# Performance work log

Hardware: AMD Instinct MI355X
Metric: run time of the kernel (lower is better)

The kernel has to match this reference:

```python
import math
import jax, jax.numpy as jnp
import numpy as np

D, H, L, DFF, V = 512, 8, 6, 2048, 32000
B, S = 2, 2048
PAD = 1


def _layernorm(x, g, b, eps=1e-5):
    m = x.mean(-1, keepdims=True)
    v = ((x - m) ** 2).mean(-1, keepdims=True)
    return (x - m) / jnp.sqrt(v + eps) * g + b


def _mha(qx, kx, w, b, mask, h=H):
    # w: [4, D, D] (q,k,v,out), b: [4, D]; mask broadcastable to [B,1,Sq,Sk]
    bs, sq, d = qx.shape
    dk = d // h
    def proj(x, i):
        return (x @ w[i] + b[i]).reshape(bs, -1, h, dk).transpose(0, 2, 1, 3)
    q, k, v = proj(qx, 0), proj(kx, 1), proj(kx, 2)
    scores = jnp.einsum('bhqd,bhkd->bhqk', q, k) / math.sqrt(dk)
    scores = jnp.where(mask, scores, -jnp.inf)
    attn = jax.nn.softmax(scores, axis=-1)
    out = jnp.einsum('bhqk,bhkd->bhqd', attn, v).transpose(0, 2, 1, 3).reshape(bs, sq, d)
    return out @ w[3] + b[3]


def _ff(x, w1, b1, w2, b2):
    return jax.nn.relu(x @ w1 + b1) @ w2 + b2


def _sinusoidal_pe(max_len, d):
    pos = np.arange(max_len)[:, None].astype(np.float64)
    div = np.exp(np.arange(0, d, 2) * (-math.log(10000.0) / d))
    pe = np.zeros((max_len, d), np.float32)
    pe[:, 0::2] = np.sin(pos * div)
    pe[:, 1::2] = np.cos(pos * div)
    return jnp.asarray(pe[None])  # [1, max_len, d]


def setup_inputs() -> dict:
    key = jax.random.key(0)
    ks = iter(jax.random.split(key, 32))
    def w(shape):
        return jax.random.normal(next(ks), shape, jnp.float32) * 0.02
    inp = {
        'src': jax.random.randint(next(ks), (B, S), 2, V),
        'tgt': jax.random.randint(next(ks), (B, S), 2, V),
        'src_emb': w((V, D)),
        'tgt_emb': w((V, D)),
        'pe': _sinusoidal_pe(S, D),
        'enc_attn_w': w((L, 4, D, D)), 'enc_attn_b': jnp.zeros((L, 4, D)),
        'enc_ff_w1': w((L, D, DFF)), 'enc_ff_b1': jnp.zeros((L, DFF)),
        'enc_ff_w2': w((L, DFF, D)), 'enc_ff_b2': jnp.zeros((L, D)),
        'enc_ln_g': jnp.ones((L, 2, D)), 'enc_ln_b': jnp.zeros((L, 2, D)),
        'dec_self_w': w((L, 4, D, D)), 'dec_self_b': jnp.zeros((L, 4, D)),
        'dec_src_w': w((L, 4, D, D)), 'dec_src_b': jnp.zeros((L, 4, D)),
        'dec_ff_w1': w((L, D, DFF)), 'dec_ff_b1': jnp.zeros((L, DFF)),
        'dec_ff_w2': w((L, DFF, D)), 'dec_ff_b2': jnp.zeros((L, D)),
        'dec_ln_g': jnp.ones((L, 3, D)), 'dec_ln_b': jnp.zeros((L, 3, D)),
        'ln_g': jnp.ones((D,)), 'ln_b': jnp.zeros((D,)),
        'fc_w': w((D, V)), 'fc_b': jnp.zeros((V,)),
    }
    return inp


def reference(src, tgt, src_emb, tgt_emb, pe,
              enc_attn_w, enc_attn_b, enc_ff_w1, enc_ff_b1, enc_ff_w2, enc_ff_b2,
              enc_ln_g, enc_ln_b,
              dec_self_w, dec_self_b, dec_src_w, dec_src_b,
              dec_ff_w1, dec_ff_b1, dec_ff_w2, dec_ff_b2, dec_ln_g, dec_ln_b,
              ln_g, ln_b, fc_w, fc_b):
    s_len, t_len = src.shape[1], tgt.shape[1]
    src_mask = (src != PAD)[:, None, None, :]                      # [B,1,1,Ss]
    tril = jnp.tril(jnp.ones((t_len, t_len), bool))
    tgt_mask = (tgt != PAD)[:, None, None, :] & tril[None, None]   # [B,1,St,St]

    x = src_emb[src] + pe[:, :s_len]
    for l in range(L):
        x2 = _layernorm(x, enc_ln_g[l, 0], enc_ln_b[l, 0])
        x = x + _mha(x2, x2, enc_attn_w[l], enc_attn_b[l], src_mask)
        x2 = _layernorm(x, enc_ln_g[l, 1], enc_ln_b[l, 1])
        x = x + _ff(x2, enc_ff_w1[l], enc_ff_b1[l], enc_ff_w2[l], enc_ff_b2[l])
    memory = x

    y = tgt_emb[tgt] + pe[:, :t_len]
    for l in range(L):
        y2 = _layernorm(y, dec_ln_g[l, 0], dec_ln_b[l, 0])
        y = y + _mha(y2, y2, dec_self_w[l], dec_self_b[l], tgt_mask)
        y2 = _layernorm(y, dec_ln_g[l, 1], dec_ln_b[l, 1])
        y = y + _mha(y2, memory, dec_src_w[l], dec_src_b[l], src_mask)
        y2 = _layernorm(y, dec_ln_g[l, 2], dec_ln_b[l, 2])
        y = y + _ff(y2, dec_ff_w1[l], dec_ff_b1[l], dec_ff_w2[l], dec_ff_b2[l])

    return _layernorm(y, ln_g, ln_b) @ fc_w + fc_b  # [B, St, V]
```

## Files before the change

kernel.cpp:

```cpp
#include <hip/hip_runtime.h>
#include <math.h>

#define D_MODEL 512
#define NHEAD   8
#define NLAYER  6
#define DFF_    2048
#define VOCAB   32000
#define BATCH   2
#define SEQ     2048
#define NTOK    (BATCH*SEQ)
#define PAD_ID  1

typedef __attribute__((ext_vector_type(8))) short s16x8;
typedef __attribute__((ext_vector_type(4))) float f32x4;
typedef unsigned short u16;
typedef unsigned int   u32;
typedef unsigned long long u64;

__device__ __forceinline__ u16 f2bf(float x) {
  u32 u = __builtin_bit_cast(u32, x);
  u += 0x7FFFu + ((u >> 16) & 1u);
  return (u16)(u >> 16);
}

__device__ __forceinline__ float exp2i(float x) {
  float r; asm("v_exp_f32 %0, %1" : "=v"(r) : "v"(x)); return r;
}

__device__ __forceinline__ void gload16(const void* g, void* l) {
  __builtin_amdgcn_global_load_lds(
      (const __attribute__((address_space(1))) u32*)g,
      (__attribute__((address_space(3))) u32*)l, 16, 0, 0);
}

#define CEXP 0.1803368802f

__global__ __launch_bounds__(256) void embed_kernel(
    const int* __restrict__ tok, const float* __restrict__ emb,
    const float* __restrict__ pe, float* __restrict__ out)
{
  const int total = NTOK * D_MODEL;
  for (int i = blockIdx.x * 256 + threadIdx.x; i < total; i += gridDim.x * 256) {
    int t = i >> 9;
    int d = i & 511;
    int s = t & (SEQ - 1);
    out[i] = emb[(size_t)tok[t] * D_MODEL + d] + pe[(size_t)s * D_MODEL + d];
  }
}

__global__ __launch_bounds__(64) void padmask_kernel(
    const int* __restrict__ tok, u64* __restrict__ pm)
{
  int b = blockIdx.y, t = blockIdx.x;
  int lane = threadIdx.x;
  u64 m = __ballot(tok[(size_t)b * SEQ + t * 64 + lane] != PAD_ID);
  if (lane == 0) pm[b * (SEQ / 64) + t] = m;
}

__global__ __launch_bounds__(256) void ln_kernel(
    const float* __restrict__ x, const float* __restrict__ g,
    const float* __restrict__ bb, u16* __restrict__ y)
{
  __shared__ float red[8];
  const size_t row = blockIdx.x;
  const float* xr = x + row * D_MODEL;
  u16* yr = y + row * D_MODEL;
  const int t = threadIdx.x;
  float a0 = xr[t], a1 = xr[t + 256];
  float s = a0 + a1;
  #pragma unroll
  for (int o = 32; o > 0; o >>= 1) s += __shfl_down(s, o, 64);
  int wv = t >> 6, ln = t & 63;
  if (ln == 0) red[wv] = s;
  __syncthreads();
  if (t == 0) red[4] = red[0] + red[1] + red[2] + red[3];
  __syncthreads();
  float mean = red[4] * (1.0f / D_MODEL);
  float d0 = a0 - mean, d1 = a1 - mean;
  float vs = d0 * d0 + d1 * d1;
  #pragma unroll
  for (int o = 32; o > 0; o >>= 1) vs += __shfl_down(vs, o, 64);
  if (ln == 0) red[wv] = vs;
  __syncthreads();
  if (t == 0) red[5] = red[0] + red[1] + red[2] + red[3];
  __syncthreads();
  float inv = rsqrtf(red[5] * (1.0f / D_MODEL) + 1e-5f);
  yr[t]       = f2bf(d0 * inv * g[t]       + bb[t]);
  yr[t + 256] = f2bf(d1 * inv * g[t + 256] + bb[t + 256]);
}

__global__ __launch_bounds__(256) void cvtbf_kernel(
    const float* __restrict__ s, u16* __restrict__ d, int n)
{
  int i = (blockIdx.x * 256 + threadIdx.x) * 8;
  if (i >= n) return;
  float4 a = *(const float4*)&s[i];
  float4 b = *(const float4*)&s[i + 4];
  u32 p0 = (u32)f2bf(a.x) | ((u32)f2bf(a.y) << 16);
  u32 p1 = (u32)f2bf(a.z) | ((u32)f2bf(a.w) << 16);
  u32 p2 = (u32)f2bf(b.x) | ((u32)f2bf(b.y) << 16);
  u32 p3 = (u32)f2bf(b.z) | ((u32)f2bf(b.w) << 16);
  uint4 o; o.x = p0; o.y = p1; o.z = p2; o.w = p3;
  *(uint4*)&d[i] = o;
}

__global__ __launch_bounds__(256) void tconv_kernel(
    const float* __restrict__ src, u16* __restrict__ dst, int K, int N)
{
  __shared__ float tile[64][65];
  const size_t z = blockIdx.z;
  src += z * (size_t)K * N;
  dst += z * (size_t)K * N;
  const int n0 = blockIdx.x * 64, k0 = blockIdx.y * 64;
  const int t = threadIdx.x;
  const int cr = t >> 4, cc = (t & 15) * 4;
  #pragma unroll
  for (int it = 0; it < 4; ++it) {
    int kr = cr + it * 16;
    float4 v = *(const float4*)&src[(size_t)(k0 + kr) * N + n0 + cc];
    tile[kr][cc] = v.x; tile[kr][cc + 1] = v.y; tile[kr][cc + 2] = v.z; tile[kr][cc + 3] = v.w;
  }
  __syncthreads();
  #pragma unroll
  for (int it = 0; it < 4; ++it) {
    int nr = cr + it * 16;
    u32 lo = (u32)f2bf(tile[cc + 0][nr]) | ((u32)f2bf(tile[cc + 1][nr]) << 16);
    u32 hi = (u32)f2bf(tile[cc + 2][nr]) | ((u32)f2bf(tile[cc + 3][nr]) << 16);
    uint2 pk; pk.x = lo; pk.y = hi;
    *(uint2*)&dst[(size_t)(n0 + nr) * K + k0 + cc] = pk;
  }
}

template<int MODE, int BM, int BN, int MAP>
__global__ __launch_bounds__(256, 2) void mm_kernel(
    const u16* __restrict__ A, const u16* __restrict__ Wt,
    const float* __restrict__ bias, const float* __restrict__ res,
    void* __restrict__ Cout, u16* __restrict__ vtOut,
    int M, int N, int K,
    long long wStride, long long bStride, long long cStride)
{
  constexpr int MI = BM / 32;
  constexpr int NI = BN / 32;
  __shared__ u16 sh[(BM + BN) * 64];
  u16* As = sh;
  u16* Bs = sh + BM * 64;
  const int z = blockIdx.z;
  size_t wOff, bOff;
  if (MAP == 1) {
    wOff = (size_t)(z >> 1) * 4 * 262144 + (size_t)(1 + (z & 1)) * 262144;
    bOff = (size_t)(z >> 1) * 4 * 512 + (size_t)(1 + (z & 1)) * 512;
  } else {
    wOff = (size_t)z * wStride;
    bOff = (size_t)z * bStride;
  }
  Wt += wOff;
  bias += bOff;
  const int bm = blockIdx.y * BM, bn = blockIdx.x * BN;
  const int tid = threadIdx.x, lane = tid & 63, w = tid >> 6;
  const int wm = w >> 1, wn = w & 1;
  const int l15 = lane & 15, l4 = lane >> 4;
  const int wrow0 = wm * (BM / 2), wcol0 = wn * (BN / 2);
  const u16* aBase = A  + (size_t)bm * K;
  const u16* bBase = Wt + (size_t)bn * K;
  f32x4 acc[MI][NI] = {};

  for (int k0 = 0; k0 < K; k0 += 64) {
    #pragma unroll
    for (int i = 0; i < BM / 32; ++i) {
      int lin = i * 256 + tid;
      int r = lin >> 3, sp = lin & 7;
      gload16(aBase + (size_t)r * K + k0 + ((sp ^ (r & 7)) * 8), &As[(i * 256 + w * 64) * 8]);
    }
    #pragma unroll
    for (int i = 0; i < BN / 32; ++i) {
      int lin = i * 256 + tid;
      int r = lin >> 3, sp = lin & 7;
      gload16(bBase + (size_t)r * K + k0 + ((sp ^ (r & 7)) * 8), &Bs[(i * 256 + w * 64) * 8]);
    }
    __syncthreads();
    #pragma unroll
    for (int ks = 0; ks < 2; ++ks) {
      s16x8 af[MI], bf[NI];
      #pragma unroll
      for (int mi = 0; mi < MI; ++mi) {
        int rr = wrow0 + mi * 16 + l15;
        af[mi] = *(const s16x8*)&As[(rr << 6) + (((ks * 4 + l4) ^ (rr & 7)) << 3)];
      }
      #pragma unroll
      for (int ni = 0; ni < NI; ++ni) {
        int rr = wcol0 + ni * 16 + l15;
        bf[ni] = *(const s16x8*)&Bs[(rr << 6) + (((ks * 4 + l4) ^ (rr & 7)) << 3)];
      }
      #pragma unroll
      for (int mi = 0; mi < MI; ++mi)
        #pragma unroll
        for (int ni = 0; ni < NI; ++ni)
          acc[mi][ni] = __builtin_amdgcn_mfma_f32_16x16x32_bf16(af[mi], bf[ni], acc[mi][ni], 0, 0, 0);
    }
    __syncthreads();
  }

  const bool vpath = (MODE == 4 && z == 2) || (MODE == 5 && (z & 1) == 1);
  if (vpath) {
    u16* TT = sh;
    #pragma unroll
    for (int mi = 0; mi < MI; ++mi)
      #pragma unroll
      for (int ni = 0; ni < NI; ++ni)
        #pragma unroll
        for (int r = 0; r < 4; ++r) {
          int rowl = wrow0 + mi * 16 + l4 * 4 + r;
          int coll = wcol0 + ni * 16 + l15;
          TT[coll * 72 + rowl] = f2bf(acc[mi][ni][r] + bias[bn + coll]);
        }
    __syncthreads();
    const int b = bm >> 11, s0loc = bm & 2047, h = bn >> 6;
    const int layer = (MODE == 5) ? (z >> 1) : 0;
    u16* vbase = vtOut + (size_t)layer * ((size_t)NTOK * D_MODEL)
               + ((size_t)(b * NHEAD + h) * 64) * SEQ;
    int d = tid >> 2, sc = (tid & 3) * 16;
    s16x8 v0 = *(const s16x8*)&TT[d * 72 + sc];
    s16x8 v1 = *(const s16x8*)&TT[d * 72 + sc + 8];
    *(s16x8*)(vbase + (size_t)d * SEQ + s0loc + sc) = v0;
    *(s16x8*)(vbase + (size_t)d * SEQ + s0loc + sc + 8) = v1;
    return;
  }

  const int zi = (MAP == 1) ? (z >> 1) : z;
  #pragma unroll
  for (int ni = 0; ni < NI; ++ni) {
    int col = bn + wcol0 + ni * 16 + l15;
    float bb = bias[col];
    #pragma unroll
    for (int mi = 0; mi < MI; ++mi) {
      #pragma unroll
      for (int r = 0; r < 4; ++r) {
        int row = bm + wrow0 + mi * 16 + l4 * 4 + r;
        size_t off = (size_t)zi * cStride + (size_t)row * N + col;
        float v = acc[mi][ni][r] + bb;
        if (MODE == 1) v += res[(size_t)row * N + col];
        if (MODE == 3) v = fmaxf(v, 0.0f);
        if (MODE <= 1) ((float*)Cout)[off] = v;
        else           ((u16*)Cout)[off] = f2bf(v);
      }
    }
  }
}

template<int CAUSAL>
__global__ __launch_bounds__(256, 2) void fattn_kernel(
    const u16* __restrict__ Qg, const u16* __restrict__ Kg,
    const u16* __restrict__ Vt, const u64* __restrict__ padm,
    u16* __restrict__ Og)
{
  __shared__ u16 Ks[2][128 * 64];
  __shared__ u16 Vs[2][64 * 128];
  __shared__ u16 Ps[4][16 * 128];
  const int qtile = CAUSAL ? (int)(gridDim.x - 1 - blockIdx.x) : (int)blockIdx.x;
  const int qt = qtile * 64;
  const int h = blockIdx.y, b = blockIdx.z;
  const int tid = threadIdx.x, lane = tid & 63, w = tid >> 6;
  const int l15 = lane & 15, l4 = lane >> 4;
  const int hoff = h * 64;
  const u16* Kbase = Kg + (size_t)(b * SEQ) * D_MODEL + hoff;
  const u16* Vbase = Vt + (size_t)(b * NHEAD + h) * 64 * SEQ;
  const u64* pmb = padm + b * (SEQ / 64);

  s16x8 aq[2];
  {
    const u16* qp = Qg + (size_t)(b * SEQ + qt + w * 16 + l15) * D_MODEL + hoff + l4 * 8;
    aq[0] = *(const s16x8*)qp;
    aq[1] = *(const s16x8*)(qp + 32);
  }

  f32x4 oacc[4] = {};
  float mrow[4] = {-1e30f, -1e30f, -1e30f, -1e30f};
  float lrow[4] = {0.f, 0.f, 0.f, 0.f};
  const int nt = CAUSAL ? (qt >> 7) + 1 : SEQ / 128;

  #define STAGE(KV0, BUF)                                                              \
    {                                                                                  \
      _Pragma("unroll")                                                                \
      for (int it = 0; it < 4; ++it) {                                                 \
        int lin = it * 256 + tid;                                                      \
        int rr = lin >> 3, sp = lin & 7;                                               \
        gload16(Kbase + (size_t)((KV0) + rr) * D_MODEL + ((sp ^ (rr & 7)) * 8),        \
                &Ks[BUF][(it * 256 + w * 64) * 8]);                                    \
      }                                                                                \
      _Pragma("unroll")                                                                \
      for (int it = 0; it < 4; ++it) {                                                 \
        int lin = it * 256 + tid;                                                      \
        int rr = lin >> 4, ko = lin & 15;                                              \
        gload16(Vbase + (size_t)rr * SEQ + (KV0) + ((ko ^ (rr & 15)) * 8),             \
                &Vs[BUF][(it * 256 + w * 64) * 8]);                                    \
      }                                                                                \
    }

  STAGE(0, 0);
  __syncthreads();

  for (int kt = 0; kt < nt; ++kt) {
    const int kv0 = kt * 128;
    const int cur = kt & 1;
    if (kt + 1 < nt) STAGE(kv0 + 128, cur ^ 1);

    f32x4 sac[8] = {};
    #pragma unroll
    for (int ks = 0; ks < 2; ++ks)
      #pragma unroll
      for (int jn = 0; jn < 8; ++jn) {
        int rr = jn * 16 + l15;
        s16x8 bk = *(const s16x8*)&Ks[cur][(rr << 6) + (((ks * 4 + l4) ^ (rr & 7)) << 3)];
        sac[jn] = __builtin_amdgcn_mfma_f32_16x16x32_bf16(aq[ks], bk, sac[jn], 0, 0, 0);
      }

    const u64 m0 = pmb[(kv0 >> 6)];
    const u64 m1 = pmb[(kv0 >> 6) + 1];
    const bool lastC = CAUSAL && (kt == nt - 1);
    if (((m0 & m1) != ~0ull) || lastC) {
      #pragma unroll
      for (int jn = 0; jn < 8; ++jn) {
        int kvg = kv0 + jn * 16 + l15;
        u64 mm = (jn < 4) ? m0 : m1;
        bool okp = (mm >> ((jn & 3) * 16 + l15)) & 1;
        #pragma unroll
        for (int r = 0; r < 4; ++r) {
// ... 55 lines not shown
    }
    __syncthreads();
  }
  #undef STAGE

  float inv[4];
  #pragma unroll
  for (int r = 0; r < 4; ++r) inv[r] = 1.0f / lrow[r];
  #pragma unroll
  for (int jn = 0; jn < 4; ++jn)
    #pragma unroll
    for (int r = 0; r < 4; ++r)
      Og[(size_t)(b * SEQ + qt + w * 16 + l4 * 4 + r) * D_MODEL + hoff + jn * 16 + l15] =
          f2bf(oacc[jn][r] * inv[r]);
}

extern "C" void kernel_launch(void* const* d_in, const int* in_sizes, int n_in,
                              void* d_out, int out_size, void* d_ws, size_t ws_size,
                              hipStream_t stream)
{
  const int*   src        = (const int*)  d_in[0];
  const int*   tgt        = (const int*)  d_in[1];
  const float* src_emb    = (const float*)d_in[2];
  const float* tgt_emb    = (const float*)d_in[3];
  const float* pe         = (const float*)d_in[4];
  const float* enc_attn_w = (const float*)d_in[5];
  const float* enc_attn_b = (const float*)d_in[6];
  const float* enc_ff_w1  = (const float*)d_in[7];
  const float* enc_ff_b1  = (const float*)d_in[8];
  const float* enc_ff_w2  = (const float*)d_in[9];
  const float* enc_ff_b2  = (const float*)d_in[10];
  const float* enc_ln_g   = (const float*)d_in[11];
  const float* enc_ln_bb  = (const float*)d_in[12];
  const float* dec_self_w = (const float*)d_in[13];
  const float* dec_self_b = (const float*)d_in[14];
  const float* dec_src_w  = (const float*)d_in[15];
  const float* dec_src_b  = (const float*)d_in[16];
  const float* dec_ff_w1  = (const float*)d_in[17];
  const float* dec_ff_b1  = (const float*)d_in[18];
  const float* dec_ff_w2  = (const float*)d_in[19];
  const float* dec_ff_b2  = (const float*)d_in[20];
  const float* dec_ln_g   = (const float*)d_in[21];
  const float* dec_ln_bb  = (const float*)d_in[22];
  const float* fin_ln_g   = (const float*)d_in[23];
  const float* fin_ln_b   = (const float*)d_in[24];
  const float* fc_w       = (const float*)d_in[25];
  const float* fc_b       = (const float*)d_in[26];
  float* out = (float*)d_out;

  const size_t DD = (size_t)D_MODEL * D_MODEL;
  const size_t FD = (size_t)D_MODEL * DFF_;
  const size_t TD = (size_t)NTOK * D_MODEL;

  char* ob = (char*)d_out;
  size_t off = 0;
  auto alloco = [&](size_t bytes) { void* p = ob + off; off += (bytes + 255) & ~(size_t)255; return p; };
  u16* wt_enc_attn = (u16*)alloco(24 * DD * 2);
  u16* wt_dec_self = (u16*)alloco(24 * DD * 2);
  u16* wt_dec_src  = (u16*)alloco(24 * DD * 2);
  u16* wt_enc_ff1  = (u16*)alloco(6 * FD * 2);
  u16* wt_enc_ff2  = (u16*)alloco(6 * FD * 2);
  u16* wt_dec_ff1  = (u16*)alloco(6 * FD * 2);
  u16* wt_dec_ff2  = (u16*)alloco(6 * FD * 2);
  u16* qb   = (u16*)alloco(2 * TD * 2);
  u16* kb   = qb + TD;
  u16* vtb  = (u16*)alloco(TD * 2);
  u16* aob  = (u16*)alloco(TD * 2);
  u16* hbb  = (u16*)alloco((size_t)NTOK * DFF_ * 2);
  u16* memb = (u16*)alloco(TD * 2);
  u16* ckb  = (u16*)alloco(6 * TD * 2);
  u16* cvtb = (u16*)alloco(6 * TD * 2);

  char* wsb = (char*)d_ws;
  u16*   fcwt = (u16*)wsb;
  size_t wo = ((size_t)VOCAB * D_MODEL * 2 + 255) & ~(size_t)255;
  float* xe  = (float*)(wsb + wo); wo += TD * 4;
  float* yd  = (float*)(wsb + wo); wo += TD * 4;
  u16*   x2b = (u16*)(wsb + wo);   wo += TD * 2;
  u64*   pmS = (u64*)(wsb + wo);   wo += 1024;
  u64*   pmT = (u64*)(wsb + wo);

  dim3 blk(256);
  dim3 gN512(8, 64, 1), gQKV(8, 64, 3), gCKV(8, 64, 12);
  dim3 gFF1(16, 32, 1), gFF2(8, 64, 1), gFC(250, 32, 1);
  dim3 gAttn(SEQ / 64, NHEAD, BATCH);
  dim3 gPM(SEQ / 64, BATCH);
  const long long llDD = (long long)DD, llTD = (long long)TD;

  padmask_kernel<<<gPM, dim3(64), 0, stream>>>(src, pmS);
  padmask_kernel<<<gPM, dim3(64), 0, stream>>>(tgt, pmT);
  tconv_kernel<<<dim3(8, 8, 24), blk, 0, stream>>>(enc_attn_w, wt_enc_attn, 512, 512);
  tconv_kernel<<<dim3(8, 8, 24), blk, 0, stream>>>(dec_self_w, wt_dec_self, 512, 512);
  tconv_kernel<<<dim3(8, 8, 24), blk, 0, stream>>>(dec_src_w,  wt_dec_src,  512, 512);
  tconv_kernel<<<dim3(32, 8, 6), blk, 0, stream>>>(enc_ff_w1, wt_enc_ff1, 512, 2048);
  tconv_kernel<<<dim3(8, 32, 6), blk, 0, stream>>>(enc_ff_w2, wt_enc_ff2, 2048, 512);
  tconv_kernel<<<dim3(32, 8, 6), blk, 0, stream>>>(dec_ff_w1, wt_dec_ff1, 512, 2048);
  tconv_kernel<<<dim3(8, 32, 6), blk, 0, stream>>>(dec_ff_w2, wt_dec_ff2, 2048, 512);
  tconv_kernel<<<dim3(500, 8, 1), blk, 0, stream>>>(fc_w, fcwt, 512, VOCAB);

  embed_kernel<<<dim3(2048), blk, 0, stream>>>(src, src_emb, pe, xe);
  for (int l = 0; l < NLAYER; ++l) {
    ln_kernel<<<dim3(NTOK), blk, 0, stream>>>(xe, enc_ln_g + (size_t)(l * 2 + 0) * D_MODEL,
                                              enc_ln_bb + (size_t)(l * 2 + 0) * D_MODEL, x2b);
    mm_kernel<4, 64, 64, 0><<<gQKV, blk, 0, stream>>>(x2b, wt_enc_attn + (size_t)l * 4 * DD,
        enc_attn_b + (size_t)l * 4 * D_MODEL, nullptr, qb, vtb, NTOK, 512, 512, llDD, D_MODEL, llTD);
    fattn_kernel<0><<<gAttn, blk, 0, stream>>>(qb, kb, vtb, pmS, aob);
    mm_kernel<1, 64, 64, 0><<<gN512, blk, 0, stream>>>(aob, wt_enc_attn + (size_t)(l * 4 + 3) * DD,
        enc_attn_b + (size_t)(l * 4 + 3) * D_MODEL, xe, xe, nullptr, NTOK, 512, 512, 0, 0, 0);
    ln_kernel<<<dim3(NTOK), blk, 0, stream>>>(xe, enc_ln_g + (size_t)(l * 2 + 1) * D_MODEL,
                                              enc_ln_bb + (size_t)(l * 2 + 1) * D_MODEL, x2b);
    mm_kernel<3, 128, 128, 0><<<gFF1, blk, 0, stream>>>(x2b, wt_enc_ff1 + (size_t)l * FD,
        enc_ff_b1 + (size_t)l * DFF_, nullptr, hbb, nullptr, NTOK, DFF_, 512, 0, 0, 0);
    mm_kernel<1, 64, 64, 0><<<gFF2, blk, 0, stream>>>(hbb, wt_enc_ff2 + (size_t)l * FD,
        enc_ff_b2 + (size_t)l * D_MODEL, xe, xe, nullptr, NTOK, 512, DFF_, 0, 0, 0);
  }
  cvtbf_kernel<<<dim3(1024), blk, 0, stream>>>(xe, memb, NTOK * D_MODEL);

  mm_kernel<5, 64, 64, 1><<<gCKV, blk, 0, stream>>>(memb, wt_dec_src, dec_src_b, nullptr,
      ckb, cvtb, NTOK, 512, 512, 0, 0, llTD);

  embed_kernel<<<dim3(2048), blk, 0, stream>>>(tgt, tgt_emb, pe, yd);
  for (int l = 0; l < NLAYER; ++l) {
    const u16* Ws = wt_dec_self + (size_t)l * 4 * DD;
    const u16* Wc = wt_dec_src + (size_t)l * 4 * DD;
    const float* bs  = dec_self_b + (size_t)l * 4 * D_MODEL;
    const float* bcb = dec_src_b + (size_t)l * 4 * D_MODEL;
    ln_kernel<<<dim3(NTOK), blk, 0, stream>>>(yd, dec_ln_g + (size_t)(l * 3 + 0) * D_MODEL,
                                              dec_ln_bb + (size_t)(l * 3 + 0) * D_MODEL, x2b);
    mm_kernel<4, 64, 64, 0><<<gQKV, blk, 0, stream>>>(x2b, Ws, bs, nullptr, qb, vtb,
                                                      NTOK, 512, 512, llDD, D_MODEL, llTD);
    fattn_kernel<1><<<gAttn, blk, 0, stream>>>(qb, kb, vtb, pmT, aob);
    mm_kernel<1, 64, 64, 0><<<gN512, blk, 0, stream>>>(aob, Ws + 3 * DD, bs + 3 * D_MODEL, yd, yd,
                                                       nullptr, NTOK, 512, 512, 0, 0, 0);
    ln_kernel<<<dim3(NTOK), blk, 0, stream>>>(yd, dec_ln_g + (size_t)(l * 3 + 1) * D_MODEL,
                                              dec_ln_bb + (size_t)(l * 3 + 1) * D_MODEL, x2b);
    mm_kernel<2, 64, 64, 0><<<gN512, blk, 0, stream>>>(x2b, Wc, bcb, nullptr, qb, nullptr,
                                                       NTOK, 512, 512, 0, 0, 0);
    fattn_kernel<0><<<gAttn, blk, 0, stream>>>(qb, ckb + (size_t)l * TD, cvtb + (size_t)l * TD,
                                               pmS, aob);
    mm_kernel<1, 64, 64, 0><<<gN512, blk, 0, stream>>>(aob, Wc + 3 * DD, bcb + 3 * D_MODEL, yd, yd,
                                                       nullptr, NTOK, 512, 512, 0, 0, 0);
    ln_kernel<<<dim3(NTOK), blk, 0, stream>>>(yd, dec_ln_g + (size_t)(l * 3 + 2) * D_MODEL,
                                              dec_ln_bb + (size_t)(l * 3 + 2) * D_MODEL, x2b);
    mm_kernel<3, 128, 128, 0><<<gFF1, blk, 0, stream>>>(x2b, wt_dec_ff1 + (size_t)l * FD,
        dec_ff_b1 + (size_t)l * DFF_, nullptr, hbb, nullptr, NTOK, DFF_, 512, 0, 0, 0);
    mm_kernel<1, 64, 64, 0><<<gFF2, blk, 0, stream>>>(hbb, wt_dec_ff2 + (size_t)l * FD,
        dec_ff_b2 + (size_t)l * D_MODEL, yd, yd, nullptr, NTOK, 512, DFF_, 0, 0, 0);
  }

  ln_kernel<<<dim3(NTOK), blk, 0, stream>>>(yd, fin_ln_g, fin_ln_b, x2b);
  mm_kernel<0, 128, 128, 0><<<gFC, blk, 0, stream>>>(x2b, fcwt, fc_b, nullptr, out, nullptr,
                                                     NTOK, VOCAB, 512, 0, 0, 0);

  (void)in_sizes; (void)n_in; (void)out_size; (void)ws_size;
}
```

Baseline: 2.516 ms.

## Fuse LayerNorm into following GEMMs and batch setup kernels

```diff
diff --git a/kernel.cpp b/kernel.cpp
--- a/kernel.cpp
+++ b/kernel.cpp
@@ -35,10 +35,15 @@
 
 #define CEXP 0.1803368802f
 
-__global__ __launch_bounds__(256) void embed_kernel(
-    const int* __restrict__ tok, const float* __restrict__ emb,
-    const float* __restrict__ pe, float* __restrict__ out)
-{
+__global__ __launch_bounds__(256) void embed2_kernel(
+    const int* __restrict__ src, const int* __restrict__ tgt,
+    const float* __restrict__ se, const float* __restrict__ te,
+    const float* __restrict__ pe, float* __restrict__ xe, float* __restrict__ yd)
+{
+  const int z = blockIdx.y;
+  const int* tok = z ? tgt : src;
+  const float* emb = z ? te : se;
+  float* out = z ? yd : xe;
   const int total = NTOK * D_MODEL;
   for (int i = blockIdx.x * 256 + threadIdx.x; i < total; i += gridDim.x * 256) {
     int t = i >> 9;
@@ -48,9 +53,13 @@
   }
 }
 
-__global__ __launch_bounds__(64) void padmask_kernel(
-    const int* __restrict__ tok, u64* __restrict__ pm)
-{
+__global__ __launch_bounds__(64) void padmask2_kernel(
+    const int* __restrict__ src, const int* __restrict__ tgt,
+    u64* __restrict__ pmS, u64* __restrict__ pmT)
+{
+  const int z = blockIdx.z;
+  const int* tok = z ? tgt : src;
+  u64* pm = z ? pmT : pmS;
   int b = blockIdx.y, t = blockIdx.x;
   int lane = threadIdx.x;
   u64 m = __ballot(tok[(size_t)b * SEQ + t * 64 + lane] != PAD_ID);
@@ -89,28 +98,14 @@
   yr[t + 256] = f2bf(d1 * inv * g[t + 256] + bb[t + 256]);
 }
 
-__global__ __launch_bounds__(256) void cvtbf_kernel(
-    const float* __restrict__ s, u16* __restrict__ d, int n)
-{
-  int i = (blockIdx.x * 256 + threadIdx.x) * 8;
-  if (i >= n) return;
-  float4 a = *(const float4*)&s[i];
-  float4 b = *(const float4*)&s[i + 4];
-  u32 p0 = (u32)f2bf(a.x) | ((u32)f2bf(a.y) << 16);
-  u32 p1 = (u32)f2bf(a.z) | ((u32)f2bf(a.w) << 16);
-  u32 p2 = (u32)f2bf(b.x) | ((u32)f2bf(b.y) << 16);
-  u32 p3 = (u32)f2bf(b.z) | ((u32)f2bf(b.w) << 16);
-  uint4 o; o.x = p0; o.y = p1; o.z = p2; o.w = p3;
-  *(uint4*)&d[i] = o;
-}
-
-__global__ __launch_bounds__(256) void tconv_kernel(
-    const float* __restrict__ src, u16* __restrict__ dst, int K, int N)
+__global__ __launch_bounds__(256) void tconv2_kernel(
+    const float* __restrict__ s0, const float* __restrict__ s1,
+    u16* __restrict__ d0, u16* __restrict__ d1, int zsplit, int K, int N)
 {
   __shared__ float tile[64][65];
-  const size_t z = blockIdx.z;
-  src += z * (size_t)K * N;
-  dst += z * (size_t)K * N;
+  const int z = blockIdx.z;
+  const float* src = (z < zsplit) ? s0 + (size_t)z * K * N : s1 + (size_t)(z - zsplit) * K * N;
+  u16* dst = (z < zsplit) ? d0 + (size_t)z * K * N : d1 + (size_t)(z - zsplit) * K * N;
   const int n0 = blockIdx.x * 64, k0 = blockIdx.y * 64;
   const int t = threadIdx.x;
   const int cr = t >> 4, cc = (t & 15) * 4;
@@ -128,6 +123,139 @@
     u32 hi = (u32)f2bf(tile[cc + 2][nr]) | ((u32)f2bf(tile[cc + 3][nr]) << 16);
     uint2 pk; pk.x = lo; pk.y = hi;
     *(uint2*)&dst[(size_t)(n0 + nr) * K + k0 + cc] = pk;
+  }
+}
+
+template<int MODE>
+__global__ __launch_bounds__(256, 2) void mmln_kernel(
+    const float* __restrict__ Xf, const float* __restrict__ lng,
+    const float* __restrict__ lnb, const u16* __restrict__ Wt,
+    const float* __restrict__ bias, u16* __restrict__ Cout,
+    u16* __restrict__ vtOut, int N,
+    long long wStride, long long bStride, long long cStride)
+{
+  __shared__ u16 Ap[64 * 512];
+  __shared__ u16 Bs[2][64 * 64];
+  const int z = blockIdx.z;
+  Wt   += (size_t)z * wStride;
+  bias += (size_t)z * bStride;
+  const int bm = blockIdx.y * 64, bn = blockIdx.x * 64;
+  const int tid = threadIdx.x, lane = tid & 63, w = tid >> 6;
+  const int wm = w >> 1, wn = w & 1;
+  const int l15 = lane & 15, l4 = lane >> 4;
+  const u16* bBase = Wt + (size_t)bn * 512;
+
+  #define STAGE_B(K0, BUF)                                                    \
+    { _Pragma("unroll")                                                       \
+      for (int i = 0; i < 2; ++i) {                                           \
+        int lin = i * 256 + tid;                                              \
+        int rr2 = lin >> 3, sp = lin & 7;                                     \
+        gload16(bBase + (size_t)rr2 * 512 + (K0) + ((sp ^ (rr2 & 7)) * 8),    \
+                &Bs[BUF][(i * 256 + w * 64) * 8]);                            \
+      } }
+
+  STAGE_B(0, 0);
+
+  const int r = tid >> 2, q = tid & 3;
+  const float* xrow = Xf + (size_t)(bm + r) * 512 + q * 128;
+  float sum = 0.f, ss = 0.f;
+  #pragma unroll
+  for (int i = 0; i < 32; ++i) {
+    float4 v = *(const float4*)&xrow[i * 4];
+    sum += (v.x + v.y) + (v.z + v.w);
+    ss  += v.x * v.x + v.y * v.y + v.z * v.z + v.w * v.w;
+  }
+  sum += __shfl_xor(sum, 1, 4); sum += __shfl_xor(sum, 2, 4);
+  ss  += __shfl_xor(ss, 1, 4);  ss  += __shfl_xor(ss, 2, 4);
+  float mean = sum * (1.0f / 512.0f);
+  float inv = rsqrtf(ss * (1.0f / 512.0f) - mean * mean + 1e-5f);
+  #pragma unroll
+  for (int g8 = 0; g8 < 16; ++g8) {
+    int col0 = q * 128 + g8 * 8;
+    float4 a = *(const float4*)&xrow[g8 * 8];
+    float4 b = *(const float4*)&xrow[g8 * 8 + 4];
+    float4 g0 = *(const float4*)&lng[col0];
+    float4 g1 = *(const float4*)&lng[col0 + 4];
+    float4 c0 = *(const float4*)&lnb[col0];
+    float4 c1 = *(const float4*)&lnb[col0 + 4];
+    s16x8 ev;
+    ev[0] = (short)f2bf((a.x - mean) * inv * g0.x + c0.x);
+    ev[1] = (short)f2bf((a.y - mean) * inv * g0.y + c0.y);
+    ev[2] = (short)f2bf((a.z - mean) * inv * g0.z + c0.z);
+    ev[3] = (short)f2bf((a.w - mean) * inv * g0.w + c0.w);
+    ev[4] = (short)f2bf((b.x - mean) * inv * g1.x + c1.x);
+    ev[5] = (short)f2bf((b.y - mean) * inv * g1.y + c1.y);
+    ev[6] = (short)f2bf((b.z - mean) * inv * g1.z + c1.z);
+    ev[7] = (short)f2bf((b.w - mean) * inv * g1.w + c1.w);
+    int kg = col0 >> 3;
+    *(s16x8*)&Ap[(r << 9) + ((kg ^ (r & 7)) << 3)] = ev;
+  }
+  __syncthreads();
+
+  f32x4 acc[2][2] = {};
+  for (int k0 = 0; k0 < 512; k0 += 64) {
+    const int cur = (k0 >> 6) & 1;
+    if (k0 < 448) STAGE_B(k0 + 64, cur ^ 1);
+    #pragma unroll
+    for (int ks = 0; ks < 2; ++ks) {
+      s16x8 af[2], bf[2];
+      #pragma unroll
+      for (int mi = 0; mi < 2; ++mi) {
+        int rr = wm * 32 + mi * 16 + l15;
+        af[mi] = *(const s16x8*)&Ap[(rr << 9) + ((((k0 >> 3) + ks * 4 + l4) ^ (rr & 7)) << 3)];
+      }
+      #pragma unroll
+      for (int ni = 0; ni < 2; ++ni) {
+        int rr = wn * 32 + ni * 16 + l15;
+        bf[ni] = *(const s16x8*)&Bs[cur][(rr << 6) + (((ks * 4 + l4) ^ (rr & 7)) << 3)];
+      }
+      #pragma unroll
+      for (int mi = 0; mi < 2; ++mi)
+        #pragma unroll
+        for (int ni = 0; ni < 2; ++ni)
+          acc[mi][ni] = __builtin_amdgcn_mfma_f32_16x16x32_bf16(af[mi], bf[ni], acc[mi][ni], 0, 0, 0);
+    }
+    __syncthreads();
+  }
+  #undef STAGE_B
+
+  if (MODE == 2 && z == 2) {
+    u16* TT = Ap;
+    #pragma unroll
+    for (int mi = 0; mi < 2; ++mi)
+      #pragma unroll
+      for (int ni = 0; ni < 2; ++ni)
+        #pragma unroll
+        for (int rr = 0; rr < 4; ++rr) {
+          int rowl = wm * 32 + mi * 16 + l4 * 4 + rr;
+          int coll = wn * 32 + ni * 16 + l15;
+          TT[coll * 72 + rowl] = f2bf(acc[mi][ni][rr] + bias[bn + coll]);
+        }
+    __syncthreads();
+    const int b = bm >> 11, s0loc = bm & 2047, h = bn >> 6;
+    u16* vbase = vtOut + ((size_t)(b * NHEAD + h) * 64) * SEQ;
+    int d = tid >> 2, sc = (tid & 3) * 16;
+    s16x8 v0 = *(const s16x8*)&TT[d * 72 + sc];
+    s16x8 v1 = *(const s16x8*)&TT[d * 72 + sc + 8];
+    *(s16x8*)(vbase + (size_t)d * SEQ + s0loc + sc) = v0;
+    *(s16x8*)(vbase + (size_t)d * SEQ + s0loc + sc + 8) = v1;
+    return;
+  }
+
+  #pragma unroll
+  for (int ni = 0; ni < 2; ++ni) {
+    int col = bn + wn * 32 + ni * 16 + l15;
+    float bb = bias[col];
+    #pragma unroll
+    for (int mi = 0; mi < 2; ++mi) {
+      #pragma unroll
+      for (int rr = 0; rr < 4; ++rr) {
+        int row = bm + wm * 32 + mi * 16 + l4 * 4 + rr;
+        float v = acc[mi][ni][rr] + bb;
+        if (MODE == 1) v = fmaxf(v, 0.0f);
+        Cout[(size_t)z * cStride + (size_t)row * N + col] = f2bf(v);
+      }
+    }
   }
 }
 
@@ -200,7 +328,7 @@
     __syncthreads();
   }
 
-  const bool vpath = (MODE == 4 && z == 2) || (MODE == 5 && (z & 1) == 1);
+  const bool vpath = (MODE == 5 && (z & 1) == 1);
   if (vpath) {
     u16* TT = sh;
     #pragma unroll
@@ -215,7 +343,7 @@
         }
     __syncthreads();
     const int b = bm >> 11, s0loc = bm & 2047, h = bn >> 6;
-    const int layer = (MODE == 5) ? (z >> 1) : 0;
+    const int layer = z >> 1;
     u16* vbase = vtOut + (size_t)layer * ((size_t)NTOK * D_MODEL)
                + ((size_t)(b * NHEAD + h) * 64) * SEQ;
     int d = tid >> 2, sc = (tid & 3) * 16;
@@ -238,10 +366,10 @@
         int row = bm + wrow0 + mi * 16 + l4 * 4 + r;
         size_t off = (size_t)zi * cStride + (size_t)row * N + col;
         float v = acc[mi][ni][r] + bb;
-        if (MODE == 1) v += res[(size_t)row * N + col];
-        if (MODE == 3) v = fmaxf(v, 0.0f);
-        if (MODE <= 1) ((float*)Cout)[off] = v;
-        else           ((u16*)Cout)[off] = f2bf(v);
+        if (MODE == 1 || MODE == 6) v += res[(size_t)row * N + col];
+        if (MODE <= 1 || MODE == 6) ((float*)Cout)[off] = v;
+        else                        ((u16*)Cout)[off] = f2bf(v);
+        if (MODE == 6) vtOut[(size_t)row * N + col] = f2bf(v);
       }
     }
   }
@@ -463,69 +591,64 @@
 
   dim3 blk(256);
   dim3 gN512(8, 64, 1), gQKV(8, 64, 3), gCKV(8, 64, 12);
-  dim3 gFF1(16, 32, 1), gFF2(8, 64, 1), gFC(250, 32, 1);
+  dim3 gFF1(32, 64, 1), gFC(250, 32, 1);
   dim3 gAttn(SEQ / 64, NHEAD, BATCH);
-  dim3 gPM(SEQ / 64, BATCH);
   const long long llDD = (long long)DD, llTD = (long long)TD;
 
-  padmask_kernel<<<gPM, dim3(64), 0, stream>>>(src, pmS);
-  padmask_kernel<<<gPM, dim3(64), 0, stream>>>(tgt, pmT);
-  tconv_kernel<<<dim3(8, 8, 24), blk, 0, stream>>>(enc_attn_w, wt_enc_attn, 512, 512);
-  tconv_kernel<<<dim3(8, 8, 24), blk, 0, stream>>>(dec_self_w, wt_dec_self, 512, 512);
-  tconv_kernel<<<dim3(8, 8, 24), blk, 0, stream>>>(dec_src_w,  wt_dec_src,  512, 512);
-  tconv_kernel<<<dim3(32, 8, 6), blk, 0, stream>>>(enc_ff_w1, wt_enc_ff1, 512, 2048);
-  tconv_kernel<<<dim3(8, 32, 6), blk, 0, stream>>>(enc_ff_w2, wt_enc_ff2, 2048, 512);
-  tconv_kernel<<<dim3(32, 8, 6), blk, 0, stream>>>(dec_ff_w1, wt_dec_ff1, 512, 2048);
-  tconv_kernel<<<dim3(8, 32, 6), blk, 0, stream>>>(dec_ff_w2, wt_dec_ff2, 2048, 512);
-  tconv_kernel<<<dim3(500, 8, 1), blk, 0, stream>>>(fc_w, fcwt, 512, VOCAB);
-
-  embed_kernel<<<dim3(2048), blk, 0, stream>>>(src, src_emb, pe, xe);
+  padmask2_kernel<<<dim3(SEQ / 64, BATCH, 2), dim3(64), 0, stream>>>(src, tgt, pmS, pmT);
+  tconv2_kernel<<<dim3(8, 8, 48), blk, 0, stream>>>(enc_attn_w, dec_self_w, wt_enc_attn, wt_dec_self, 24, 512, 512);
+  tconv2_kernel<<<dim3(8, 8, 24), blk, 0, stream>>>(dec_src_w, dec_src_w, wt_dec_src, wt_dec_src, 24, 512, 512);
+  tconv2_kernel<<<dim3(32, 8, 12), blk, 0, stream>>>(enc_ff_w1, dec_ff_w1, wt_enc_ff1, wt_dec_ff1, 6, 512, 2048);
+  tconv2_kernel<<<dim3(8, 32, 12), blk, 0, stream>>>(enc_ff_w2, dec_ff_w2, wt_enc_ff2, wt_dec_ff2, 6, 2048, 512);
+  tconv2_kernel<<<dim3(500, 8, 1), blk, 0, stream>>>(fc_w, fc_w, fcwt, fcwt, 1, 512, VOCAB);
+  embed2_kernel<<<dim3(2048, 2), blk, 0, stream>>>(src, tgt, src_emb, tgt_emb, pe, xe, yd);
+
   for (int l = 0; l < NLAYER; ++l) {
-    ln_kernel<<<dim3(NTOK), blk, 0, stream>>>(xe, enc_ln_g + (size_t)(l * 2 + 0) * D_MODEL,
-                                              enc_ln_bb + (size_t)(l * 2 + 0) * D_MODEL, x2b);
-    mm_kernel<4, 64, 64, 0><<<gQKV, blk, 0, stream>>>(x2b, wt_enc_attn + (size_t)l * 4 * DD,
-        enc_attn_b + (size_t)l * 4 * D_MODEL, nullptr, qb, vtb, NTOK, 512, 512, llDD, D_MODEL, llTD);
+    mmln_kernel<2><<<gQKV, blk, 0, stream>>>(xe,
+        enc_ln_g + (size_t)(l * 2 + 0) * D_MODEL, enc_ln_bb + (size_t)(l * 2 + 0) * D_MODEL,
+        wt_enc_attn + (size_t)l * 4 * DD, enc_attn_b + (size_t)l * 4 * D_MODEL,
+        qb, vtb, 512, llDD, D_MODEL, llTD);
     fattn_kernel<0><<<gAttn, blk, 0, stream>>>(qb, kb, vtb, pmS, aob);
     mm_kernel<1, 64, 64, 0><<<gN512, blk, 0, stream>>>(aob, wt_enc_attn + (size_t)(l * 4 + 3) * DD,
         enc_attn_b + (size_t)(l * 4 + 3) * D_MODEL, xe, xe, nullptr, NTOK, 512, 512, 0, 0, 0);
-    ln_kernel<<<dim3(NTOK), blk, 0, stream>>>(xe, enc_ln_g + (size_t)(l * 2 + 1) * D_MODEL,
-                                              enc_ln_bb + (size_t)(l * 2 + 1) * D_MODEL, x2b);
-    mm_kernel<3, 128, 128, 0><<<gFF1, blk, 0, stream>>>(x2b, wt_enc_ff1 + (size_t)l * FD,
-        enc_ff_b1 + (size_t)l * DFF_, nullptr, hbb, nullptr, NTOK, DFF_, 512, 0, 0, 0);
-    mm_kernel<1, 64, 64, 0><<<gFF2, blk, 0, stream>>>(hbb, wt_enc_ff2 + (size_t)l * FD,
-        enc_ff_b2 + (size_t)l * D_MODEL, xe, xe, nullptr, NTOK, 512, DFF_, 0, 0, 0);
-  }
-  cvtbf_kernel<<<dim3(1024), blk, 0, stream>>>(xe, memb, NTOK * D_MODEL);
+    mmln_kernel<1><<<gFF1, blk, 0, stream>>>(xe,
+        enc_ln_g + (size_t)(l * 2 + 1) * D_MODEL, enc_ln_bb + (size_t)(l * 2 + 1) * D_MODEL,
+        wt_enc_ff1 + (size_t)l * FD, enc_ff_b1 + (size_t)l * DFF_,
+        hbb, nullptr, DFF_, 0, 0, 0);
+    if (l == NLAYER - 1)
+      mm_kernel<6, 64, 64, 0><<<gN512, blk, 0, stream>>>(hbb, wt_enc_ff2 + (size_t)l * FD,
+          enc_ff_b2 + (size_t)l * D_MODEL, xe, xe, memb, NTOK, 512, DFF_, 0, 0, 0);
+    else
+      mm_kernel<1, 64, 64, 0><<<gN512, blk, 0, stream>>>(hbb, wt_enc_ff2 + (size_t)l * FD,
+          enc_ff_b2 + (size_t)l * D_MODEL, xe, xe, nullptr, NTOK, 512, DFF_, 0, 0, 0);
+  }
 
   mm_kernel<5, 64, 64, 1><<<gCKV, blk, 0, stream>>>(memb, wt_dec_src, dec_src_b, nullptr,
       ckb, cvtb, NTOK, 512, 512, 0, 0, llTD);
 
-  embed_kernel<<<dim3(2048), blk, 0, stream>>>(tgt, tgt_emb, pe, yd);
   for (int l = 0; l < NLAYER; ++l) {
     const u16* Ws = wt_dec_self + (size_t)l * 4 * DD;
     const u16* Wc = wt_dec_src + (size_t)l * 4 * DD;
     const float* bs  = dec_self_b + (size_t)l * 4 * D_MODEL;
     const float* bcb = dec_src_b + (size_t)l * 4 * D_MODEL;
-    ln_kernel<<<dim3(NTOK), blk, 0, stream>>>(yd, dec_ln_g + (size_t)(l * 3 + 0) * D_MODEL,
-                                              dec_ln_bb + (size_t)(l * 3 + 0) * D_MODEL, x2b);
-    mm_kernel<4, 64, 64, 0><<<gQKV, blk, 0, stream>>>(x2b, Ws, bs, nullptr, qb, vtb,
-                                                      NTOK, 512, 512, llDD, D_MODEL, llTD);
+    mmln_kernel<2><<<gQKV, blk, 0, stream>>>(yd,
+        dec_ln_g + (size_t)(l * 3 + 0) * D_MODEL, dec_ln_bb + (size_t)(l * 3 + 0) * D_MODEL,
+        Ws, bs, qb, vtb, 512, llDD, D_MODEL, llTD);
     fattn_kernel<1><<<gAttn, blk, 0, stream>>>(qb, kb, vtb, pmT, aob);
     mm_kernel<1, 64, 64, 0><<<gN512, blk, 0, stream>>>(aob, Ws + 3 * DD, bs + 3 * D_MODEL, yd, yd,
                                                        nullptr, NTOK, 512, 512, 0, 0, 0);
-    ln_kernel<<<dim3(NTOK), blk, 0, stream>>>(yd, dec_ln_g + (size_t)(l * 3 + 1) * D_MODEL,
-                                              dec_ln_bb + (size_t)(l * 3 + 1) * D_MODEL, x2b);
-    mm_kernel<2, 64, 64, 0><<<gN512, blk, 0, stream>>>(x2b, Wc, bcb, nullptr, qb, nullptr,
-                                                       NTOK, 512, 512, 0, 0, 0);
+    mmln_kernel<0><<<gN512, blk, 0, stream>>>(yd,
+        dec_ln_g + (size_t)(l * 3 + 1) * D_MODEL, dec_ln_bb + (size_t)(l * 3 + 1) * D_MODEL,
+        Wc, bcb, qb, nullptr, 512, 0, 0, 0);
     fattn_kernel<0><<<gAttn, blk, 0, stream>>>(qb, ckb + (size_t)l * TD, cvtb + (size_t)l * TD,
                                                pmS, aob);
     mm_kernel<1, 64, 64, 0><<<gN512, blk, 0, stream>>>(aob, Wc + 3 * DD, bcb + 3 * D_MODEL, yd, yd,
                                                        nullptr, NTOK, 512, 512, 0, 0, 0);
-    ln_kernel<<<dim3(NTOK), blk, 0, stream>>>(yd, dec_ln_g + (size_t)(l * 3 + 2) * D_MODEL,
-                                              dec_ln_bb + (size_t)(l * 3 + 2) * D_MODEL, x2b);
-    mm_kernel<3, 128, 128, 0><<<gFF1, blk, 0, stream>>>(x2b, wt_dec_ff1 + (size_t)l * FD,
-        dec_ff_b1 + (size_t)l * DFF_, nullptr, hbb, nullptr, NTOK, DFF_, 512, 0, 0, 0);
-    mm_kernel<1, 64, 64, 0><<<gFF2, blk, 0, stream>>>(hbb, wt_dec_ff2 + (size_t)l * FD,
+    mmln_kernel<1><<<gFF1, blk, 0, stream>>>(yd,
+        dec_ln_g + (size_t)(l * 3 + 2) * D_MODEL, dec_ln_bb + (size_t)(l * 3 + 2) * D_MODEL,
+        wt_dec_ff1 + (size_t)l * FD, dec_ff_b1 + (size_t)l * DFF_,
+        hbb, nullptr, DFF_, 0, 0, 0);
+    mm_kernel<1, 64, 64, 0><<<gN512, blk, 0, stream>>>(hbb, wt_dec_ff2 + (size_t)l * FD,
         dec_ff_b2 + (size_t)l * D_MODEL, yd, yd, nullptr, NTOK, 512, DFF_, 0, 0, 0);
   }
 
```

Measured after the change: 4.759 ms. 1.89x slower.

## Double-buffer LDS in 64x64 GEMM tiles and merge small setup kernels

Applied to the files above, without the earlier changes.

```diff
diff --git a/kernel.cpp b/kernel.cpp
--- a/kernel.cpp
+++ b/kernel.cpp
@@ -35,10 +35,15 @@
 
 #define CEXP 0.1803368802f
 
-__global__ __launch_bounds__(256) void embed_kernel(
-    const int* __restrict__ tok, const float* __restrict__ emb,
-    const float* __restrict__ pe, float* __restrict__ out)
-{
+__global__ __launch_bounds__(256) void embed2_kernel(
+    const int* __restrict__ src, const int* __restrict__ tgt,
+    const float* __restrict__ se, const float* __restrict__ te,
+    const float* __restrict__ pe, float* __restrict__ xe, float* __restrict__ yd)
+{
+  const int z = blockIdx.y;
+  const int* tok = z ? tgt : src;
+  const float* emb = z ? te : se;
+  float* out = z ? yd : xe;
   const int total = NTOK * D_MODEL;
   for (int i = blockIdx.x * 256 + threadIdx.x; i < total; i += gridDim.x * 256) {
     int t = i >> 9;
@@ -48,9 +53,13 @@
   }
 }
 
-__global__ __launch_bounds__(64) void padmask_kernel(
-    const int* __restrict__ tok, u64* __restrict__ pm)
-{
+__global__ __launch_bounds__(64) void padmask2_kernel(
+    const int* __restrict__ src, const int* __restrict__ tgt,
+    u64* __restrict__ pmS, u64* __restrict__ pmT)
+{
+  const int z = blockIdx.z;
+  const int* tok = z ? tgt : src;
+  u64* pm = z ? pmT : pmS;
   int b = blockIdx.y, t = blockIdx.x;
   int lane = threadIdx.x;
   u64 m = __ballot(tok[(size_t)b * SEQ + t * 64 + lane] != PAD_ID);
@@ -89,28 +98,14 @@
   yr[t + 256] = f2bf(d1 * inv * g[t + 256] + bb[t + 256]);
 }
 
-__global__ __launch_bounds__(256) void cvtbf_kernel(
-    const float* __restrict__ s, u16* __restrict__ d, int n)
-{
-  int i = (blockIdx.x * 256 + threadIdx.x) * 8;
-  if (i >= n) return;
-  float4 a = *(const float4*)&s[i];
-  float4 b = *(const float4*)&s[i + 4];
-  u32 p0 = (u32)f2bf(a.x) | ((u32)f2bf(a.y) << 16);
-  u32 p1 = (u32)f2bf(a.z) | ((u32)f2bf(a.w) << 16);
-  u32 p2 = (u32)f2bf(b.x) | ((u32)f2bf(b.y) << 16);
-  u32 p3 = (u32)f2bf(b.z) | ((u32)f2bf(b.w) << 16);
-  uint4 o; o.x = p0; o.y = p1; o.z = p2; o.w = p3;
-  *(uint4*)&d[i] = o;
-}
-
-__global__ __launch_bounds__(256) void tconv_kernel(
-    const float* __restrict__ src, u16* __restrict__ dst, int K, int N)
+__global__ __launch_bounds__(256) void tconv2_kernel(
+    const float* __restrict__ s0, const float* __restrict__ s1,
+    u16* __restrict__ d0, u16* __restrict__ d1, int zsplit, int K, int N)
 {
   __shared__ float tile[64][65];
-  const size_t z = blockIdx.z;
-  src += z * (size_t)K * N;
-  dst += z * (size_t)K * N;
+  const int z = blockIdx.z;
+  const float* src = (z < zsplit) ? s0 + (size_t)z * K * N : s1 + (size_t)(z - zsplit) * K * N;
+  u16* dst = (z < zsplit) ? d0 + (size_t)z * K * N : d1 + (size_t)(z - zsplit) * K * N;
   const int n0 = blockIdx.x * 64, k0 = blockIdx.y * 64;
   const int t = threadIdx.x;
   const int cr = t >> 4, cc = (t & 15) * 4;
@@ -141,9 +136,8 @@
 {
   constexpr int MI = BM / 32;
   constexpr int NI = BN / 32;
-  __shared__ u16 sh[(BM + BN) * 64];
-  u16* As = sh;
-  u16* Bs = sh + BM * 64;
+  constexpr bool DB = (BM == 64 && BN == 64);
+  __shared__ u16 sh[(DB ? 2 : 1) * (BM + BN) * 64];
   const int z = blockIdx.z;
   size_t wOff, bOff;
   if (MAP == 1) {
@@ -164,32 +158,19 @@
   const u16* bBase = Wt + (size_t)bn * K;
   f32x4 acc[MI][NI] = {};
 
-  for (int k0 = 0; k0 < K; k0 += 64) {
-    #pragma unroll
-    for (int i = 0; i < BM / 32; ++i) {
-      int lin = i * 256 + tid;
-      int r = lin >> 3, sp = lin & 7;
-      gload16(aBase + (size_t)r * K + k0 + ((sp ^ (r & 7)) * 8), &As[(i * 256 + w * 64) * 8]);
-    }
-    #pragma unroll
-    for (int i = 0; i < BN / 32; ++i) {
-      int lin = i * 256 + tid;
-      int r = lin >> 3, sp = lin & 7;
-      gload16(bBase + (size_t)r * K + k0 + ((sp ^ (r & 7)) * 8), &Bs[(i * 256 + w * 64) * 8]);
-    }
-    __syncthreads();
+  auto mfma_step = [&](const u16* Asb, const u16* Bsb) {
     #pragma unroll
     for (int ks = 0; ks < 2; ++ks) {
       s16x8 af[MI], bf[NI];
       #pragma unroll
       for (int mi = 0; mi < MI; ++mi) {
         int rr = wrow0 + mi * 16 + l15;
-        af[mi] = *(const s16x8*)&As[(rr << 6) + (((ks * 4 + l4) ^ (rr & 7)) << 3)];
+        af[mi] = *(const s16x8*)&Asb[(rr << 6) + (((ks * 4 + l4) ^ (rr & 7)) << 3)];
       }
       #pragma unroll
       for (int ni = 0; ni < NI; ++ni) {
         int rr = wcol0 + ni * 16 + l15;
-        bf[ni] = *(const s16x8*)&Bs[(rr << 6) + (((ks * 4 + l4) ^ (rr & 7)) << 3)];
+        bf[ni] = *(const s16x8*)&Bsb[(rr << 6) + (((ks * 4 + l4) ^ (rr & 7)) << 3)];
       }
       #pragma unroll
       for (int mi = 0; mi < MI; ++mi)
@@ -197,7 +178,58 @@
         for (int ni = 0; ni < NI; ++ni)
           acc[mi][ni] = __builtin_amdgcn_mfma_f32_16x16x32_bf16(af[mi], bf[ni], acc[mi][ni], 0, 0, 0);
     }
+  };
+
+  if constexpr (DB) {
+    u16* As0 = sh;
+    u16* As1 = sh + 64 * 64;
+    u16* Bs0 = sh + 2 * 64 * 64;
+    u16* Bs1 = sh + 3 * 64 * 64;
+    auto stage = [&](int k0, u16* Ad, u16* Bd) {
+      #pragma unroll
+      for (int i = 0; i < 2; ++i) {
+        int lin = i * 256 + tid;
+        int r = lin >> 3, sp = lin & 7;
+        gload16(aBase + (size_t)r * K + k0 + ((sp ^ (r & 7)) * 8), &Ad[(i * 256 + w * 64) * 8]);
+      }
+      #pragma unroll
+      for (int i = 0; i < 2; ++i) {
+        int lin = i * 256 + tid;
+        int r = lin >> 3, sp = lin & 7;
+        gload16(bBase + (size_t)r * K + k0 + ((sp ^ (r & 7)) * 8), &Bd[(i * 256 + w * 64) * 8]);
+      }
+    };
+    stage(0, As0, Bs0);
     __syncthreads();
+    const int nt = K >> 6;
+    for (int t = 0; t < nt; ++t) {
+      const bool even = !(t & 1);
+      u16* Ac = even ? As0 : As1;
+      u16* Bc = even ? Bs0 : Bs1;
+      if (t + 1 < nt) stage((t + 1) << 6, even ? As1 : As0, even ? Bs1 : Bs0);
+      mfma_step(Ac, Bc);
+      __syncthreads();
+    }
+  } else {
+    u16* As = sh;
+    u16* Bs = sh + BM * 64;
+    for (int k0 = 0; k0 < K; k0 += 64) {
+      #pragma unroll
+      for (int i = 0; i < BM / 32; ++i) {
+        int lin = i * 256 + tid;
+        int r = lin >> 3, sp = lin & 7;
+        gload16(aBase + (size_t)r * K + k0 + ((sp ^ (r & 7)) * 8), &As[(i * 256 + w * 64) * 8]);
+      }
+      #pragma unroll
+      for (int i = 0; i < BN / 32; ++i) {
+        int lin = i * 256 + tid;
+        int r = lin >> 3, sp = lin & 7;
+        gload16(bBase + (size_t)r * K + k0 + ((sp ^ (r & 7)) * 8), &Bs[(i * 256 + w * 64) * 8]);
+      }
+      __syncthreads();
+      mfma_step(As, Bs);
+      __syncthreads();
+    }
   }
 
   const bool vpath = (MODE == 4 && z == 2) || (MODE == 5 && (z & 1) == 1);
@@ -238,10 +270,11 @@
         int row = bm + wrow0 + mi * 16 + l4 * 4 + r;
         size_t off = (size_t)zi * cStride + (size_t)row * N + col;
         float v = acc[mi][ni][r] + bb;
-        if (MODE == 1) v += res[(size_t)row * N + col];
+        if (MODE == 1 || MODE == 6) v += res[(size_t)row * N + col];
         if (MODE == 3) v = fmaxf(v, 0.0f);
-        if (MODE <= 1) ((float*)Cout)[off] = v;
-        else           ((u16*)Cout)[off] = f2bf(v);
+        if (MODE <= 1 || MODE == 6) ((float*)Cout)[off] = v;
+        else                        ((u16*)Cout)[off] = f2bf(v);
+        if (MODE == 6) vtOut[(size_t)row * N + col] = f2bf(v);
       }
     }
   }
@@ -463,23 +496,18 @@
 
   dim3 blk(256);
   dim3 gN512(8, 64, 1), gQKV(8, 64, 3), gCKV(8, 64, 12);
-  dim3 gFF1(16, 32, 1), gFF2(8, 64, 1), gFC(250, 32, 1);
+  dim3 gFF1(16, 32, 1), gFC(250, 32, 1);
   dim3 gAttn(SEQ / 64, NHEAD, BATCH);
-  dim3 gPM(SEQ / 64, BATCH);
   const long long llDD = (long long)DD, llTD = (long long)TD;
 
-  padmask_kernel<<<gPM, dim3(64), 0, stream>>>(src, pmS);
-  padmask_kernel<<<gPM, dim3(64), 0, stream>>>(tgt, pmT);
-  tconv_kernel<<<dim3(8, 8, 24), blk, 0, stream>>>(enc_attn_w, wt_enc_attn, 512, 512);
-  tconv_kernel<<<dim3(8, 8, 24), blk, 0, stream>>>(dec_self_w, wt_dec_self, 512, 512);
-  tconv_kernel<<<dim3(8, 8, 24), blk, 0, stream>>>(dec_src_w,  wt_dec_src,  512, 512);
-  tconv_kernel<<<dim3(32, 8, 6), blk, 0, stream>>>(enc_ff_w1, wt_enc_ff1, 512, 2048);
-  tconv_kernel<<<dim3(8, 32, 6), blk, 0, stream>>>(enc_ff_w2, wt_enc_ff2, 2048, 512);
-  tconv_kernel<<<dim3(32, 8, 6), blk, 0, stream>>>(dec_ff_w1, wt_dec_ff1, 512, 2048);
-  tconv_kernel<<<dim3(8, 32, 6), blk, 0, stream>>>(dec_ff_w2, wt_dec_ff2, 2048, 512);
-  tconv_kernel<<<dim3(500, 8, 1), blk, 0, stream>>>(fc_w, fcwt, 512, VOCAB);
-
-  embed_kernel<<<dim3(2048), blk, 0, stream>>>(src, src_emb, pe, xe);
+  padmask2_kernel<<<dim3(SEQ / 64, BATCH, 2), dim3(64), 0, stream>>>(src, tgt, pmS, pmT);
+  tconv2_kernel<<<dim3(8, 8, 48), blk, 0, stream>>>(enc_attn_w, dec_self_w, wt_enc_attn, wt_dec_self, 24, 512, 512);
+  tconv2_kernel<<<dim3(8, 8, 24), blk, 0, stream>>>(dec_src_w, dec_src_w, wt_dec_src, wt_dec_src, 24, 512, 512);
+  tconv2_kernel<<<dim3(32, 8, 12), blk, 0, stream>>>(enc_ff_w1, dec_ff_w1, wt_enc_ff1, wt_dec_ff1, 6, 512, 2048);
+  tconv2_kernel<<<dim3(8, 32, 12), blk, 0, stream>>>(enc_ff_w2, dec_ff_w2, wt_enc_ff2, wt_dec_ff2, 6, 2048, 512);
+  tconv2_kernel<<<dim3(500, 8, 1), blk, 0, stream>>>(fc_w, fc_w, fcwt, fcwt, 1, 512, VOCAB);
+  embed2_kernel<<<dim3(2048, 2), blk, 0, stream>>>(src, tgt, src_emb, tgt_emb, pe, xe, yd);
+
   for (int l = 0; l < NLAYER; ++l) {
     ln_kernel<<<dim3(NTOK), blk, 0, stream>>>(xe, enc_ln_g + (size_t)(l * 2 + 0) * D_MODEL,
                                               enc_ln_bb + (size_t)(l * 2 + 0) * D_MODEL, x2b);
@@ -492,15 +520,17 @@
                                               enc_ln_bb + (size_t)(l * 2 + 1) * D_MODEL, x2b);
     mm_kernel<3, 128, 128, 0><<<gFF1, blk, 0, stream>>>(x2b, wt_enc_ff1 + (size_t)l * FD,
         enc_ff_b1 + (size_t)l * DFF_, nullptr, hbb, nullptr, NTOK, DFF_, 512, 0, 0, 0);
-    mm_kernel<1, 64, 64, 0><<<gFF2, blk, 0, stream>>>(hbb, wt_enc_ff2 + (size_t)l * FD,
-        enc_ff_b2 + (size_t)l * D_MODEL, xe, xe, nullptr, NTOK, 512, DFF_, 0, 0, 0);
-  }
-  cvtbf_kernel<<<dim3(1024), blk, 0, stream>>>(xe, memb, NTOK * D_MODEL);
+    if (l == NLAYER - 1)
+      mm_kernel<6, 64, 64, 0><<<gN512, blk, 0, stream>>>(hbb, wt_enc_ff2 + (size_t)l * FD,
+          enc_ff_b2 + (size_t)l * D_MODEL, xe, xe, memb, NTOK, 512, DFF_, 0, 0, 0);
+    else
+      mm_kernel<1, 64, 64, 0><<<gN512, blk, 0, stream>>>(hbb, wt_enc_ff2 + (size_t)l * FD,
+          enc_ff_b2 + (size_t)l * D_MODEL, xe, xe, nullptr, NTOK, 512, DFF_, 0, 0, 0);
+  }
 
   mm_kernel<5, 64, 64, 1><<<gCKV, blk, 0, stream>>>(memb, wt_dec_src, dec_src_b, nullptr,
       ckb, cvtb, NTOK, 512, 512, 0, 0, llTD);
 
-  embed_kernel<<<dim3(2048), blk, 0, stream>>>(tgt, tgt_emb, pe, yd);
   for (int l = 0; l < NLAYER; ++l) {
     const u16* Ws = wt_dec_self + (size_t)l * 4 * DD;
     const u16* Wc = wt_dec_src + (size_t)l * 4 * DD;
@@ -525,7 +555,7 @@
                                               dec_ln_bb + (size_t)(l * 3 + 2) * D_MODEL, x2b);
     mm_kernel<3, 128, 128, 0><<<gFF1, blk, 0, stream>>>(x2b, wt_dec_ff1 + (size_t)l * FD,
         dec_ff_b1 + (size_t)l * DFF_, nullptr, hbb, nullptr, NTOK, DFF_, 512, 0, 0, 0);
-    mm_kernel<1, 64, 64, 0><<<gFF2, blk, 0, stream>>>(hbb, wt_dec_ff2 + (size_t)l * FD,
+    mm_kernel<1, 64, 64, 0><<<gN512, blk, 0, stream>>>(hbb, wt_dec_ff2 + (size_t)l * FD,
         dec_ff_b2 + (size_t)l * D_MODEL, yd, yd, nullptr, NTOK, 512, DFF_, 0, 0, 0);
   }
 
```

New measurement: 2.504 ms. Within noise of the previous version (-0.5%).
